# Kernel optimization log

Hardware: AMD Instinct MI355X
Metric: run time of the kernel (lower is better)

Reference implementation:

```python
import jax, jax.numpy as jnp
import numpy as np

NP_, NT_, NG_ = 110000, 20000, 10000  # node counts per relation graph
E = 500000                              # number of interaction records / edges
D = 64                                  # embedding_dim
F_USER, F_ITEM = 16, 16                 # engineered feature dims
NUM_LAYERS = (2, 2, 2)                  # CFG.feature_num_layers


def setup_inputs() -> dict:
    key = jax.random.key(0)
    ks = jax.random.split(key, 12)
    up_edge = jax.random.randint(ks[0], (2, E), 0, NP_, dtype=jnp.int32)
    ut_edge = jax.random.randint(ks[1], (2, E), 0, NT_, dtype=jnp.int32)
    utag_edge = jax.random.randint(ks[2], (2, E), 0, NG_, dtype=jnp.int32)
    src_feat = jax.random.normal(ks[3], (E, F_USER), dtype=jnp.float32)
    dst_feat = jax.random.normal(ks[4], (E, F_ITEM), dtype=jnp.float32)
    # xavier-uniform style embedding tables
    def xavier(k, shape):
        bound = np.sqrt(6.0 / (shape[0] + shape[1])).astype(np.float32)
        return jax.random.uniform(k, shape, jnp.float32, -bound, bound)
    up_emb = xavier(ks[5], (NP_, D))
    ut_emb = xavier(ks[6], (NT_, D))
    utag_emb = xavier(ks[7], (NG_, D))
    # feature-engineering linears (stored as [in, out]; torch does x @ W.T + b)
    W_src = jax.random.normal(ks[8], (F_USER, D), dtype=jnp.float32) / np.sqrt(F_USER)
    b_src = jnp.zeros((D,), jnp.float32)
    W_dst = jax.random.normal(ks[9], (F_ITEM, D), dtype=jnp.float32) / np.sqrt(F_ITEM)
    b_dst = jnp.zeros((D,), jnp.float32)
    return dict(up_edge=up_edge, ut_edge=ut_edge, utag_edge=utag_edge,
                src_feat=src_feat, dst_feat=dst_feat,
                up_emb=up_emb, ut_emb=ut_emb, utag_emb=utag_emb,
                W_src=W_src, b_src=b_src, W_dst=W_dst, b_dst=b_dst)


def lgconv(x, edge, n):
    # PyG LGConv: symmetric-normalized propagation, no self loops, no weights.
    src, dst = edge[0], edge[1]
    ones = jnp.ones(src.shape, x.dtype)
    deg = jax.ops.segment_sum(ones, dst, num_segments=n)
    dinv = jnp.where(deg > 0, jax.lax.rsqrt(jnp.maximum(deg, 1.0)), 0.0)
    norm = dinv[src] * dinv[dst]                      # [E]
    msg = x[src] * norm[:, None]                      # gather + scale  [E, D]
    return jax.ops.segment_sum(msg, dst, num_segments=n)  # scatter-add [N, D]


def propagate(emb, edge, n_layers):
    alpha = 1.0 / (n_layers + 1)
    x = emb
    out = emb * alpha
    for _ in range(n_layers):
        x = lgconv(x, edge, emb.shape[0])
        out = out + x * alpha
    return out


def reference(up_edge, ut_edge, utag_edge, src_feat, dst_feat,
              up_emb, ut_emb, utag_emb, W_src, b_src, W_dst, b_dst):
    fs = src_feat @ W_src + b_src                     # [E, D]
    fd = dst_feat @ W_dst + b_dst                     # [E, D]
    p = propagate(up_emb, up_edge, NUM_LAYERS[0])
    t = propagate(ut_emb, ut_edge, NUM_LAYERS[1])
    g = propagate(utag_emb, utag_edge, NUM_LAYERS[2])
    # feature_aggregation_method == 0 (sum method)
    out_src = (p[up_edge[0]] + t[ut_edge[0]] + g[utag_edge[0]]) * (1.0 / 3.0) + fs
    out_dst = (p[up_edge[1]] + t[ut_edge[1]] + g[utag_edge[1]]) * (1.0 / 3.0) + fd
    return (out_src * out_dst).sum(axis=-1)           # [E] link logits
```

## Files before the change

kernel.cpp:

```cpp
#include <hip/hip_runtime.h>

#define DIM 64
#define RNG 8
#define CHK 16
#define LDSH 14336

__device__ __forceinline__ float bf2f(unsigned short u) {
    union { unsigned int i; float f; } v; v.i = ((unsigned int)u) << 16; return v.f;
}
__device__ __forceinline__ unsigned short f2bf(float f) {
    union { float f; unsigned int i; } v; v.f = f;
    unsigned int r = v.i + 0x7fff + ((v.i >> 16) & 1);
    return (unsigned short)(r >> 16);
}
__device__ __forceinline__ float4 u2f4(ushort4 u) {
    float4 f; f.x = bf2f(u.x); f.y = bf2f(u.y); f.z = bf2f(u.z); f.w = bf2f(u.w);
    return f;
}
__device__ __forceinline__ ushort4 f2u4(float4 f) {
    ushort4 u; u.x = f2bf(f.x); u.y = f2bf(f.y); u.z = f2bf(f.z); u.w = f2bf(f.w);
    return u;
}
__device__ __forceinline__ float4 fma4(float4 a, float s, float4 c) {
    c.x = fmaf(a.x, s, c.x); c.y = fmaf(a.y, s, c.y);
    c.z = fmaf(a.z, s, c.z); c.w = fmaf(a.w, s, c.w);
    return c;
}
__device__ __forceinline__ float4 add4(float4 a, float4 b) {
    float4 r; r.x = a.x + b.x; r.y = a.y + b.y; r.z = a.z + b.z; r.w = a.w + b.w;
    return r;
}

__global__ __launch_bounds__(1024) void deg_cvt_kernel(
        const int* __restrict__ up, const int* __restrict__ ut,
        const int* __restrict__ ug, int* __restrict__ hist,
        const float4* __restrict__ e0, const float4* __restrict__ e1,
        const float4* __restrict__ e2, ushort4* __restrict__ embh,
        int NP, int NT, int NG, int NTOT, int E) {
    __shared__ int lh[LDSH];
    int b = blockIdx.x;
    const int HB = 3 * RNG * CHK;
    if (b < HB) {
        int c  = b & (CHK - 1);
        int gr = b >> 4;
        int g  = gr >> 3;
        int r  = gr & (RNG - 1);
        const int* edge = (g == 0) ? up : (g == 1) ? ut : ug;
        int nb = (g == 0) ? 0 : (g == 1) ? NP : NP + NT;
        int Ng = (g == 0) ? NP : (g == 1) ? NT : NG;
        int Q  = (Ng + RNG - 1) / RNG;
        int lo = r * Q;
        int hi = lo + Q; if (hi > Ng) hi = Ng;
        int nloc = hi - lo;
        for (int t = threadIdx.x; t < nloc; t += 1024) lh[t] = 0;
        __syncthreads();
        int CE = (E + CHK - 1) / CHK;
        int jb = c * CE, je = jb + CE; if (je > E) je = E;
        for (int j = jb + threadIdx.x; j < je; j += 1024) {
            int t = edge[E + j];
            if (t >= lo && t < hi) atomicAdd(&lh[t - lo], 1);
        }
        __syncthreads();
        for (int t = threadIdx.x; t < nloc; t += 1024)
            hist[(size_t)c * NTOT + nb + lo + t] = lh[t];
        return;
    }
    int i2 = (b - HB) * 1024 + threadIdx.x;
    int np16 = NP * 16, nt16 = NT * 16, ng16 = NG * 16;
    if (i2 >= np16 + nt16 + ng16) return;
    const float4* s; int j;
    if (i2 < np16)              { s = e0; j = i2; }
    else if (i2 < np16 + nt16)  { s = e1; j = i2 - np16; }
    else                        { s = e2; j = i2 - np16 - nt16; }
    embh[i2] = f2u4(s[j]);
}

__global__ void sumdeg_kernel(const int* __restrict__ hist, int* __restrict__ csum,
                              int* __restrict__ deg, int n) {
    int i = blockIdx.x * 256 + threadIdx.x;
    if (i >= n) return;
    int run = 0;
#pragma unroll
    for (int c = 0; c < CHK; ++c) {
        csum[(size_t)c * n + i] = run;
        run += hist[(size_t)c * n + i];
    }
    deg[i] = run;
}

__global__ void block_sums(const int* __restrict__ deg, int* __restrict__ bsum,
                           int n) {
    int i = blockIdx.x * 256 + threadIdx.x;
    int v = (i < n) ? deg[i] : 0;
#pragma unroll
    for (int s = 1; s < 64; s <<= 1) v += __shfl_xor(v, s, 64);
    __shared__ int ws[4];
    if ((threadIdx.x & 63) == 0) ws[threadIdx.x >> 6] = v;
    __syncthreads();
    if (threadIdx.x == 0) bsum[blockIdx.x] = ws[0] + ws[1] + ws[2] + ws[3];
}

__global__ void scan_bsums(int* __restrict__ bsum, int nb) {
    int lane = threadIdx.x & 63, wid = threadIdx.x >> 6;
    int v = (threadIdx.x < nb) ? bsum[threadIdx.x] : 0;
    int x = v;
#pragma unroll
    for (int s = 1; s < 64; s <<= 1) {
        int y = __shfl_up(x, s, 64);
        if (lane >= s) x += y;
    }
    __shared__ int ws[16];
    if (lane == 63) ws[wid] = x;
    __syncthreads();
    int pre = 0;
    for (int w2 = 0; w2 < wid; ++w2) pre += ws[w2];
    if (threadIdx.x < nb) bsum[threadIdx.x] = pre + x - v;
}

__global__ void scatter_offs(const int* __restrict__ deg, const int* __restrict__ bpre,
                             int* __restrict__ offs, float* __restrict__ dinv,
                             int n, int total) {
    int i = blockIdx.x * 256 + threadIdx.x;
    int lane = threadIdx.x & 63, wid = threadIdx.x >> 6;
    int v = (i < n) ? deg[i] : 0;
    int x = v;
#pragma unroll
    for (int s = 1; s < 64; s <<= 1) {
        int y = __shfl_up(x, s, 64);
        if (lane >= s) x += y;
    }
    __shared__ int ws[4];
    if (lane == 63) ws[wid] = x;
    __syncthreads();
    int pre = bpre[blockIdx.x];
    for (int w2 = 0; w2 < wid; ++w2) pre += ws[w2];
    if (i < n) {
        int e = pre + x - v;
        offs[i] = e;
        dinv[i] = (v > 0) ? rsqrtf((float)v) : 0.0f;
    }
    if (i == 0) offs[n] = total;
}

__global__ __launch_bounds__(1024) void permute3_kernel(
        const int* __restrict__ up, const int* __restrict__ ut,
        const int* __restrict__ ug, const int* __restrict__ offs,
        const int* __restrict__ csum, int* __restrict__ ei,
        int NP, int NT, int NG, int NTOT, int E) {
    __shared__ int lcur[LDSH];
    int b = blockIdx.x;
    int c  = b / 24;
    int gr = b - c * 24;
    int g  = gr >> 3;
    int r  = gr & (RNG - 1);
    const int* edge = (g == 0) ? up : (g == 1) ? ut : ug;
    int nb = (g == 0) ? 0 : (g == 1) ? NP : NP + NT;
    int Ng = (g == 0) ? NP : (g == 1) ? NT : NG;
    int Q  = (Ng + RNG - 1) / RNG;
    int lo = r * Q;
    int hi = lo + Q; if (hi > Ng) hi = Ng;
    int nloc = hi - lo;
    for (int t = threadIdx.x; t < nloc; t += 1024)
        lcur[t] = offs[nb + lo + t] + csum[(size_t)c * NTOT + nb + lo + t];
    __syncthreads();
    int CE = (E + CHK - 1) / CHK;
    int jb = c * CE, je = jb + CE; if (je > E) je = E;
    for (int j = jb + threadIdx.x; j < je; j += 1024) {
        int t = edge[E + j];
        if (t >= lo && t < hi) {
            int p = atomicAdd(&lcur[t - lo], 1);
            ei[p] = edge[j] + nb;
        }
    }
}

__global__ void conv_csr1(const int* __restrict__ offs, const int* __restrict__ ei,
                          const float* __restrict__ dinv,
                          const ushort4* __restrict__ xin, ushort4* __restrict__ xout, int N) {
    int gid = blockIdx.x * blockDim.x + threadIdx.x;
    int n = gid >> 4, l = gid & 15;
    if (n >= N) return;
    int beg = offs[n], end = offs[n + 1];
    float4 a0 = {0.f, 0.f, 0.f, 0.f}, a1 = a0, a2 = a0, a3 = a0;
    int k = beg;
    for (; k + 3 < end; k += 4) {
        int s0 = ei[k], s1 = ei[k + 1], s2 = ei[k + 2], s3 = ei[k + 3];
        float w0 = dinv[s0], w1 = dinv[s1], w2 = dinv[s2], w3 = dinv[s3];
        ushort4 u0 = xin[(size_t)s0 * 16 + l];
        ushort4 u1 = xin[(size_t)s1 * 16 + l];
        ushort4 u2 = xin[(size_t)s2 * 16 + l];
        ushort4 u3 = xin[(size_t)s3 * 16 + l];
        a0 = fma4(u2f4(u0), w0, a0);
        a1 = fma4(u2f4(u1), w1, a1);
        a2 = fma4(u2f4(u2), w2, a2);
        a3 = fma4(u2f4(u3), w3, a3);
    }
    for (; k < end; ++k) {
        int s = ei[k];
        a0 = fma4(u2f4(xin[(size_t)s * 16 + l]), dinv[s], a0);
    }
    float4 acc = add4(add4(a0, a1), add4(a2, a3));
    float sc = dinv[n];
    float4 r; r.x = acc.x * sc; r.y = acc.y * sc; r.z = acc.z * sc; r.w = acc.w * sc;
    xout[(size_t)n * 16 + l] = f2u4(r);
}

__global__ void conv_csr2(const int* __restrict__ offs, const int* __restrict__ ei,
                          const float* __restrict__ dinv,
                          const ushort4* __restrict__ emb, const ushort4* __restrict__ x1,
                          ushort4* __restrict__ out, int N) {
    int gid = blockIdx.x * blockDim.x + threadIdx.x;
    int n = gid >> 4, l = gid & 15;
    if (n >= N) return;
    int beg = offs[n], end = offs[n + 1];
    float4 a0 = {0.f, 0.f, 0.f, 0.f}, a1 = a0, a2 = a0, a3 = a0;
    int k = beg;
    for (; k + 3 < end; k += 4) {
        int s0 = ei[k], s1 = ei[k + 1], s2 = ei[k + 2], s3 = ei[k + 3];
        float w0 = dinv[s0], w1 = dinv[s1], w2 = dinv[s2], w3 = dinv[s3];
        ushort4 u0 = x1[(size_t)s0 * 16 + l];
        ushort4 u1 = x1[(size_t)s1 * 16 + l];
        ushort4 u2 = x1[(size_t)s2 * 16 + l];
        ushort4 u3 = x1[(size_t)s3 * 16 + l];
        a0 = fma4(u2f4(u0), w0, a0);
        a1 = fma4(u2f4(u1), w1, a1);
        a2 = fma4(u2f4(u2), w2, a2);
        a3 = fma4(u2f4(u3), w3, a3);
    }
    for (; k < end; ++k) {
        int s = ei[k];
        a0 = fma4(u2f4(x1[(size_t)s * 16 + l]), dinv[s], a0);
    }
    float4 acc = add4(add4(a0, a1), add4(a2, a3));
    float sc = dinv[n];
    size_t idx = (size_t)n * 16 + l;
    float4 em = u2f4(emb[idx]), x = u2f4(x1[idx]);
    const float third = 1.0f / 3.0f;
    float4 o;
    o.x = (em.x + x.x + acc.x * sc) * third;
    o.y = (em.y + x.y + acc.y * sc) * third;
    o.z = (em.z + x.z + acc.z * sc) * third;
    o.w = (em.w + x.w + acc.w * sc) * third;
    out[idx] = f2u4(o);
}

__global__ void final_kernel(const int* __restrict__ up_e, const int* __restrict__ ut_e,
                             const int* __restrict__ utag_e,
                             const float* __restrict__ src_feat, const float* __restrict__ dst_feat,
                             const ushort4* __restrict__ O,
                             const float4* __restrict__ W_s4, const float4* __restrict__ b_s4,
                             const float4* __restrict__ W_d4, const float4* __restrict__ b_d4,
                             float* __restrict__ out, int E, int NP, int NT) {
    __shared__ float4 LWs[256], LWd[256];
    int tid = threadIdx.x;
    LWs[tid] = W_s4[tid];
    LWd[tid] = W_d4[tid];
    __syncthreads();

    int gid = blockIdx.x * blockDim.x + tid;
    int grp = gid >> 4;
    int l = gid & 15;
    int e0 = grp * 4;
    if (e0 >= E) return;
    int lane = tid & 63;
    int gbase = lane & 48;

    int sp[4], dp[4], st[4], dt[4], sg[4], dg[4];
    float fsc[4], fdc[4];
#pragma unroll
    for (int j = 0; j < 4; ++j) {
        int e = e0 + j; if (e > E - 1) e = E - 1;
        sp[j] = up_e[e];              dp[j] = up_e[E + e];
        st[j] = ut_e[e] + NP;         dt[j] = ut_e[E + e] + NP;
        sg[j] = utag_e[e] + NP + NT;  dg[j] = utag_e[E + e] + NP + NT;
        fsc[j] = src_feat[(size_t)e * 16 + l];
        fdc[j] = dst_feat[(size_t)e * 16 + l];
    }
    float4 bsv = b_s4[l], bdv = b_d4[l];

    ushort4 as[4][3], bs[4][3];
#pragma unroll
    for (int j = 0; j < 4; ++j) {
        as[j][0] = O[(size_t)sp[j] * 16 + l];
        as[j][1] = O[(size_t)st[j] * 16 + l];
        as[j][2] = O[(size_t)sg[j] * 16 + l];
        bs[j][0] = O[(size_t)dp[j] * 16 + l];
        bs[j][1] = O[(size_t)dt[j] * 16 + l];
        bs[j][2] = O[(size_t)dg[j] * 16 + l];
    }

    float4 fs[4], fd[4];
#pragma unroll
    for (int j = 0; j < 4; ++j) { fs[j] = bsv; fd[j] = bdv; }

#pragma unroll
    for (int k = 0; k < 16; ++k) {
        float4 ws = LWs[k * 16 + l];
        float4 wd = LWd[k * 16 + l];
#pragma unroll
        for (int j = 0; j < 4; ++j) {
            float a = __shfl(fsc[j], gbase + k, 64);
            float c = __shfl(fdc[j], gbase + k, 64);
            fs[j] = fma4(ws, a, fs[j]);
            fd[j] = fma4(wd, c, fd[j]);
        }
    }

    const float third = 1.0f / 3.0f;
    float prod[4];
#pragma unroll
    for (int j = 0; j < 4; ++j) {
        float4 vp = u2f4(as[j][0]), vt = u2f4(as[j][1]), vg = u2f4(as[j][2]);
        float4 P, Q;
        P.x = (vp.x + vt.x + vg.x) * third + fs[j].x;
        P.y = (vp.y + vt.y + vg.y) * third + fs[j].y;
        P.z = (vp.z + vt.z + vg.z) * third + fs[j].z;
        P.w = (vp.w + vt.w + vg.w) * third + fs[j].w;
        vp = u2f4(bs[j][0]); vt = u2f4(bs[j][1]); vg = u2f4(bs[j][2]);
        Q.x = (vp.x + vt.x + vg.x) * third + fd[j].x;
        Q.y = (vp.y + vt.y + vg.y) * third + fd[j].y;
        Q.z = (vp.z + vt.z + vg.z) * third + fd[j].z;
        Q.w = (vp.w + vt.w + vg.w) * third + fd[j].w;
        float p = P.x * Q.x + P.y * Q.y + P.z * Q.z + P.w * Q.w;
        p += __shfl_xor(p, 8, 64);
        p += __shfl_xor(p, 4, 64);
        p += __shfl_xor(p, 2, 64);
        p += __shfl_xor(p, 1, 64);
        prod[j] = p;
    }
    if (l == 0) {
#pragma unroll
        for (int j = 0; j < 4; ++j)
            if (e0 + j < E) out[e0 + j] = prod[j];
    }
}

extern "C" void kernel_launch(void* const* d_in, const int* in_sizes, int n_in,
                              void* d_out, int out_size, void* d_ws, size_t ws_size,
                              hipStream_t stream) {
    const int*   up_e     = (const int*)d_in[0];
    const int*   ut_e     = (const int*)d_in[1];
    const int*   utag_e   = (const int*)d_in[2];
    const float* src_feat = (const float*)d_in[3];
    const float* dst_feat = (const float*)d_in[4];
    const float* up_emb   = (const float*)d_in[5];
    const float* ut_emb   = (const float*)d_in[6];
    const float* utag_emb = (const float*)d_in[7];
    const float* W_src    = (const float*)d_in[8];
    const float* b_src    = (const float*)d_in[9];
    const float* W_dst    = (const float*)d_in[10];
    const float* b_dst    = (const float*)d_in[11];
    float* out = (float*)d_out;

    const int E  = in_sizes[0] / 2;
    const int NP = in_sizes[5] / DIM;
    const int NT = in_sizes[6] / DIM;
    const int NG = in_sizes[7] / DIM;
    const int NTOT = NP + NT + NG;
    const int NB = (NTOT + 255) / 256;

    char* w = (char*)d_ws;
    int*  hist = (int*)w;                       w += (size_t)CHK * NTOT * 4;
    int*  csum = (int*)w;                       w += (size_t)CHK * NTOT * 4;
    int*  deg  = (int*)w;                       w += (size_t)NTOT * 4;
    int*  offs = (int*)w;                       w += (size_t)(NTOT + 1) * 4;
    int*  bsum = (int*)w;                       w += (size_t)1024 * 4;
    float* dinv = (float*)w;                    w += (size_t)NTOT * 4;
    w = (char*)(((uintptr_t)w + 127) & ~(uintptr_t)127);
    int*  ei   = (int*)w;                       w += (size_t)3 * E * 4;
    w = (char*)(((uintptr_t)w + 127) & ~(uintptr_t)127);
    ushort4* embh = (ushort4*)w;                w += (size_t)NTOT * 16 * 8;
    ushort4* x1h  = (ushort4*)w;                w += (size_t)NTOT * 16 * 8;
    ushort4* outh = (ushort4*)w;

    const int BT = 256;
    const int HB = 3 * RNG * CHK;

    {
        int convBlocks = (NTOT * 16 + 1023) / 1024;
        deg_cvt_kernel<<<dim3(HB + convBlocks), dim3(1024), 0, stream>>>(
            up_e, ut_e, utag_e, hist,
            (const float4*)up_emb, (const float4*)ut_emb, (const float4*)utag_emb,
            embh, NP, NT, NG, NTOT, E);
    }

    sumdeg_kernel<<<dim3(NB), dim3(BT), 0, stream>>>(hist, csum, deg, NTOT);

    block_sums<<<dim3(NB), dim3(BT), 0, stream>>>(deg, bsum, NTOT);
    scan_bsums<<<dim3(1), dim3(1024), 0, stream>>>(bsum, NB);
    scatter_offs<<<dim3(NB), dim3(BT), 0, stream>>>(deg, bsum, offs, dinv, NTOT, 3 * E);

    permute3_kernel<<<dim3(CHK * 24), dim3(1024), 0, stream>>>(
        up_e, ut_e, utag_e, offs, csum, ei, NP, NT, NG, NTOT, E);

    int nb = ((size_t)NTOT * 16 + BT - 1) / BT;
    conv_csr1<<<dim3(nb), dim3(BT), 0, stream>>>(offs, ei, dinv, embh, x1h, NTOT);
    conv_csr2<<<dim3(nb), dim3(BT), 0, stream>>>(offs, ei, dinv, embh, x1h, outh, NTOT);

    long long groups = (E + 3) / 4;
    final_kernel<<<dim3((groups * 16 + BT - 1) / BT), dim3(BT), 0, stream>>>(
        up_e, ut_e, utag_e, src_feat, dst_feat, outh,
        (const float4*)W_src, (const float4*)b_src,
        (const float4*)W_dst, (const float4*)b_dst, out, E, NP, NT);
}
```

Before: 332.6 us.

## Compute feature linears in final kernel with bf16 MFMA instead of shuffle FMAs

The per-edge feature projections (16->64 linears) in the final kernel move from a shuffle-and-FMA loop to bf16 MFMA 16x16x16 instructions. The weights are pre-packed into MFMA B-fragment layout by an extra block in the first kernel. Each wave now handles 16 edges, with lanes remapped so the gathers line up with the MFMA output layout. This removes shuffle and FMA work and the LDS weight staging, at the cost of rounding the features and weights to bf16.

```diff
diff --git a/kernel.cpp b/kernel.cpp
--- a/kernel.cpp
+++ b/kernel.cpp
@@ -4,6 +4,9 @@
 #define RNG 8
 #define CHK 16
 #define LDSH 14336
+
+typedef __attribute__((ext_vector_type(4))) short s16x4;
+typedef __attribute__((ext_vector_type(4))) float f32x4v;
 
 __device__ __forceinline__ float bf2f(unsigned short u) {
     union { unsigned int i; float f; } v; v.i = ((unsigned int)u) << 16; return v.f;
@@ -36,6 +39,8 @@
         const int* __restrict__ ug, int* __restrict__ hist,
         const float4* __restrict__ e0, const float4* __restrict__ e1,
         const float4* __restrict__ e2, ushort4* __restrict__ embh,
+        const float* __restrict__ W_s, const float* __restrict__ W_d,
+        s16x4* __restrict__ wfrag,
         int NP, int NT, int NG, int NTOT, int E) {
     __shared__ int lh[LDSH];
     int b = blockIdx.x;
@@ -63,6 +68,23 @@
         __syncthreads();
         for (int t = threadIdx.x; t < nloc; t += 1024)
             hist[(size_t)c * NTOT + nb + lo + t] = lh[t];
+        return;
+    }
+    int convBlocks = (NTOT * 16 + 1023) / 1024;
+    if (b >= HB + convBlocks) {
+        int i = threadIdx.x;
+        if (i < 512) {
+            int m = i >> 8;
+            int t = (i >> 6) & 3;
+            int l = i & 63;
+            int q = l >> 4, cc = l & 15;
+            const float* Wm = m ? W_d : W_s;
+            s16x4 v;
+#pragma unroll
+            for (int j = 0; j < 4; ++j)
+                v[j] = (short)f2bf(Wm[(4 * q + j) * 64 + 4 * cc + t]);
+            wfrag[i] = v;
+        }
         return;
     }
     int i2 = (b - HB) * 1024 + threadIdx.x;
@@ -244,94 +266,89 @@
     out[idx] = f2u4(o);
 }
 
-__global__ void final_kernel(const int* __restrict__ up_e, const int* __restrict__ ut_e,
-                             const int* __restrict__ utag_e,
-                             const float* __restrict__ src_feat, const float* __restrict__ dst_feat,
-                             const ushort4* __restrict__ O,
-                             const float4* __restrict__ W_s4, const float4* __restrict__ b_s4,
-                             const float4* __restrict__ W_d4, const float4* __restrict__ b_d4,
-                             float* __restrict__ out, int E, int NP, int NT) {
-    __shared__ float4 LWs[256], LWd[256];
+__global__ __launch_bounds__(256) void final_kernel(
+        const int* __restrict__ up_e, const int* __restrict__ ut_e,
+        const int* __restrict__ utag_e,
+        const float* __restrict__ src_feat, const float* __restrict__ dst_feat,
+        const ushort4* __restrict__ O, const s16x4* __restrict__ wfrag,
+        const float4* __restrict__ b_s4, const float4* __restrict__ b_d4,
+        float* __restrict__ out, int E, int NP, int NT) {
     int tid = threadIdx.x;
-    LWs[tid] = W_s4[tid];
-    LWd[tid] = W_d4[tid];
-    __syncthreads();
-
-    int gid = blockIdx.x * blockDim.x + tid;
-    int grp = gid >> 4;
-    int l = gid & 15;
-    int e0 = grp * 4;
-    if (e0 >= E) return;
-    int lane = tid & 63;
-    int gbase = lane & 48;
-
-    int sp[4], dp[4], st[4], dt[4], sg[4], dg[4];
-    float fsc[4], fdc[4];
-#pragma unroll
-    for (int j = 0; j < 4; ++j) {
-        int e = e0 + j; if (e > E - 1) e = E - 1;
-        sp[j] = up_e[e];              dp[j] = up_e[E + e];
-        st[j] = ut_e[e] + NP;         dt[j] = ut_e[E + e] + NP;
-        sg[j] = utag_e[e] + NP + NT;  dg[j] = utag_e[E + e] + NP + NT;
-        fsc[j] = src_feat[(size_t)e * 16 + l];
-        fdc[j] = dst_feat[(size_t)e * 16 + l];
-    }
-    float4 bsv = b_s4[l], bdv = b_d4[l];
+    int wv = tid >> 6;
+    int l  = tid & 63;
+    int c  = l & 15;
+    int q  = l >> 4;
+    int e0w = (blockIdx.x * 4 + wv) * 16;
+    if (e0w >= E) return;
+
+    int ea = e0w + c; if (ea > E - 1) ea = E - 1;
+    float4 fa = *(const float4*)(src_feat + (size_t)ea * 16 + q * 4);
+    float4 ga = *(const float4*)(dst_feat + (size_t)ea * 16 + q * 4);
+
+    s16x4 Bs[4], Bd[4];
+#pragma unroll
+    for (int t = 0; t < 4; ++t) {
+        Bs[t] = wfrag[t * 64 + l];
+        Bd[t] = wfrag[256 + t * 64 + l];
+    }
+    float4 bsv = b_s4[c], bdv = b_d4[c];
+
+    s16x4 As, Ad;
+    As[0] = (short)f2bf(fa.x); As[1] = (short)f2bf(fa.y);
+    As[2] = (short)f2bf(fa.z); As[3] = (short)f2bf(fa.w);
+    Ad[0] = (short)f2bf(ga.x); Ad[1] = (short)f2bf(ga.y);
+    Ad[2] = (short)f2bf(ga.z); Ad[3] = (short)f2bf(ga.w);
 
     ushort4 as[4][3], bs[4][3];
 #pragma unroll
-    for (int j = 0; j < 4; ++j) {
-        as[j][0] = O[(size_t)sp[j] * 16 + l];
-        as[j][1] = O[(size_t)st[j] * 16 + l];
-        as[j][2] = O[(size_t)sg[j] * 16 + l];
-        bs[j][0] = O[(size_t)dp[j] * 16 + l];
-        bs[j][1] = O[(size_t)dt[j] * 16 + l];
-        bs[j][2] = O[(size_t)dg[j] * 16 + l];
-    }
-
-    float4 fs[4], fd[4];
-#pragma unroll
-    for (int j = 0; j < 4; ++j) { fs[j] = bsv; fd[j] = bdv; }
-
-#pragma unroll
-    for (int k = 0; k < 16; ++k) {
-        float4 ws = LWs[k * 16 + l];
-        float4 wd = LWd[k * 16 + l];
-#pragma unroll
-        for (int j = 0; j < 4; ++j) {
-            float a = __shfl(fsc[j], gbase + k, 64);
-            float c = __shfl(fdc[j], gbase + k, 64);
-            fs[j] = fma4(ws, a, fs[j]);
-            fd[j] = fma4(wd, c, fd[j]);
-        }
+    for (int r = 0; r < 4; ++r) {
+        int e = e0w + q * 4 + r; if (e > E - 1) e = E - 1;
+        int sp = up_e[e],             dp = up_e[E + e];
+        int st = ut_e[e] + NP,        dt = ut_e[E + e] + NP;
+        int sg = utag_e[e] + NP + NT, dg = utag_e[E + e] + NP + NT;
+        as[r][0] = O[(size_t)sp * 16 + c];
+        as[r][1] = O[(size_t)st * 16 + c];
+        as[r][2] = O[(size_t)sg * 16 + c];
+        bs[r][0] = O[(size_t)dp * 16 + c];
+        bs[r][1] = O[(size_t)dt * 16 + c];
+        bs[r][2] = O[(size_t)dg * 16 + c];
+    }
+    __builtin_amdgcn_sched_barrier(0);
+
+    f32x4v Cs[4], Cd[4];
+    f32x4v zz = {0.f, 0.f, 0.f, 0.f};
+#pragma unroll
+    for (int t = 0; t < 4; ++t) {
+        Cs[t] = __builtin_amdgcn_mfma_f32_16x16x16bf16_1k(As, Bs[t], zz, 0, 0, 0);
+        Cd[t] = __builtin_amdgcn_mfma_f32_16x16x16bf16_1k(Ad, Bd[t], zz, 0, 0, 0);
     }
 
     const float third = 1.0f / 3.0f;
-    float prod[4];
-#pragma unroll
-    for (int j = 0; j < 4; ++j) {
-        float4 vp = u2f4(as[j][0]), vt = u2f4(as[j][1]), vg = u2f4(as[j][2]);
+#pragma unroll
+    for (int r = 0; r < 4; ++r) {
+        int er = e0w + q * 4 + r;
+        float4 fsv, fdv;
+        fsv.x = Cs[0][r] + bsv.x; fsv.y = Cs[1][r] + bsv.y;
+        fsv.z = Cs[2][r] + bsv.z; fsv.w = Cs[3][r] + bsv.w;
+        fdv.x = Cd[0][r] + bdv.x; fdv.y = Cd[1][r] + bdv.y;
+        fdv.z = Cd[2][r] + bdv.z; fdv.w = Cd[3][r] + bdv.w;
+        float4 vp = u2f4(as[r][0]), vt = u2f4(as[r][1]), vg = u2f4(as[r][2]);
         float4 P, Q;
-        P.x = (vp.x + vt.x + vg.x) * third + fs[j].x;
-        P.y = (vp.y + vt.y + vg.y) * third + fs[j].y;
-        P.z = (vp.z + vt.z + vg.z) * third + fs[j].z;
-        P.w = (vp.w + vt.w + vg.w) * third + fs[j].w;
-        vp = u2f4(bs[j][0]); vt = u2f4(bs[j][1]); vg = u2f4(bs[j][2]);
-        Q.x = (vp.x + vt.x + vg.x) * third + fd[j].x;
-        Q.y = (vp.y + vt.y + vg.y) * third + fd[j].y;
-        Q.z = (vp.z + vt.z + vg.z) * third + fd[j].z;
-        Q.w = (vp.w + vt.w + vg.w) * third + fd[j].w;
+        P.x = (vp.x + vt.x + vg.x) * third + fsv.x;
+        P.y = (vp.y + vt.y + vg.y) * third + fsv.y;
+        P.z = (vp.z + vt.z + vg.z) * third + fsv.z;
+        P.w = (vp.w + vt.w + vg.w) * third + fsv.w;
+        vp = u2f4(bs[r][0]); vt = u2f4(bs[r][1]); vg = u2f4(bs[r][2]);
+        Q.x = (vp.x + vt.x + vg.x) * third + fdv.x;
+        Q.y = (vp.y + vt.y + vg.y) * third + fdv.y;
+        Q.z = (vp.z + vt.z + vg.z) * third + fdv.z;
+        Q.w = (vp.w + vt.w + vg.w) * third + fdv.w;
         float p = P.x * Q.x + P.y * Q.y + P.z * Q.z + P.w * Q.w;
         p += __shfl_xor(p, 8, 64);
         p += __shfl_xor(p, 4, 64);
         p += __shfl_xor(p, 2, 64);
         p += __shfl_xor(p, 1, 64);
-        prod[j] = p;
-    }
-    if (l == 0) {
-#pragma unroll
-        for (int j = 0; j < 4; ++j)
-            if (e0 + j < E) out[e0 + j] = prod[j];
+        if (c == 0 && er < E) out[er] = p;
     }
 }
 
@@ -367,6 +384,8 @@
     int*  bsum = (int*)w;                       w += (size_t)1024 * 4;
     float* dinv = (float*)w;                    w += (size_t)NTOT * 4;
     w = (char*)(((uintptr_t)w + 127) & ~(uintptr_t)127);
+    s16x4* wfrag = (s16x4*)w;                   w += (size_t)512 * 8;
+    w = (char*)(((uintptr_t)w + 127) & ~(uintptr_t)127);
     int*  ei   = (int*)w;                       w += (size_t)3 * E * 4;
     w = (char*)(((uintptr_t)w + 127) & ~(uintptr_t)127);
     ushort4* embh = (ushort4*)w;                w += (size_t)NTOT * 16 * 8;
@@ -378,10 +397,10 @@
 
     {
         int convBlocks = (NTOT * 16 + 1023) / 1024;
-        deg_cvt_kernel<<<dim3(HB + convBlocks), dim3(1024), 0, stream>>>(
+        deg_cvt_kernel<<<dim3(HB + convBlocks + 1), dim3(1024), 0, stream>>>(
             up_e, ut_e, utag_e, hist,
             (const float4*)up_emb, (const float4*)ut_emb, (const float4*)utag_emb,
-            embh, NP, NT, NG, NTOT, E);
+            embh, W_src, W_dst, wfrag, NP, NT, NG, NTOT, E);
     }
 
     sumdeg_kernel<<<dim3(NB), dim3(BT), 0, stream>>>(hist, csum, deg, NTOT);
@@ -397,9 +416,10 @@
     conv_csr1<<<dim3(nb), dim3(BT), 0, stream>>>(offs, ei, dinv, embh, x1h, NTOT);
     conv_csr2<<<dim3(nb), dim3(BT), 0, stream>>>(offs, ei, dinv, embh, x1h, outh, NTOT);
 
-    long long groups = (E + 3) / 4;
-    final_kernel<<<dim3((groups * 16 + BT - 1) / BT), dim3(BT), 0, stream>>>(
-        up_e, ut_e, utag_e, src_feat, dst_feat, outh,
-        (const float4*)W_src, (const float4*)b_src,
-        (const float4*)W_dst, (const float4*)b_dst, out, E, NP, NT);
-}
+    {
+        int blocks = (E + 63) / 64;
+        final_kernel<<<dim3(blocks), dim3(BT), 0, stream>>>(
+            up_e, ut_e, utag_e, src_feat, dst_feat, outh, wfrag,
+            (const float4*)b_src, (const float4*)b_dst, out, E, NP, NT);
+    }
+}
```

Result: no change. 329.1 us (-1.1%).
